# Optimization experiments

Measured on AMD Instinct MI355X. Metric: run time of the kernel, lower is better.

Reference implementation:

```python
import jax, jax.numpy as jnp
import numpy as np

EPS = 1e-6
RATIO = 0.5


def lrelu(x):
    return jnp.where(x > 0, x, 0.1 * x)


def conv1x1(x, w, b):
    # x (B,Ci,H,W), w (Co,Ci)
    return jnp.einsum('bihw,oi->bohw', x, w) + b[None, :, None, None]


def conv3x3(x, w, b, groups=1):
    y = jax.lax.conv_general_dilated(x, w, (1, 1), [(1, 1), (1, 1)],
        dimension_numbers=('NCHW', 'OIHW', 'NCHW'), feature_group_count=groups)
    return y + b[None, :, None, None]


def ln_cf(x, w, b):
    # channels-first LayerNorm over dim 1 (matches custom LayerNorm in source)
    u = x.mean(1, keepdims=True)
    s = ((x - u) ** 2).mean(1, keepdims=True)
    xn = (x - u) / jnp.sqrt(s + EPS)
    return w[None, :, None, None] * xn + b[None, :, None, None]


def flow_warp(x, flow):
    # bilinear warp, align_corners=True, zeros padding; flow (B,H,W,2): ch0=col offset, ch1=row offset (pixels)
    B, C, H, W = x.shape
    sx = jnp.arange(W, dtype=x.dtype)[None, None, :] + flow[..., 0]
    sy = jnp.arange(H, dtype=x.dtype)[None, :, None] + flow[..., 1]
    x0 = jnp.floor(sx)
    y0 = jnp.floor(sy)
    flat = x.reshape(B, C, H * W)

    def gather(xi, yi):
        valid = ((xi >= 0) & (xi <= W - 1) & (yi >= 0) & (yi <= H - 1)).astype(x.dtype)
        xc = jnp.clip(xi, 0, W - 1).astype(jnp.int32)
        yc = jnp.clip(yi, 0, H - 1).astype(jnp.int32)
        idx = (yc * W + xc).reshape(B, H * W)
        g = jnp.take_along_axis(flat, idx[:, None, :], axis=2).reshape(B, C, H, W)
        return g * valid[:, None, :, :]

    wx = sx - x0
    wy = sy - y0
    return (gather(x0, y0) * ((1 - wx) * (1 - wy))[:, None]
            + gather(x0 + 1, y0) * (wx * (1 - wy))[:, None]
            + gather(x0, y0 + 1) * ((1 - wx) * wy)[:, None]
            + gather(x0 + 1, y0 + 1) * (wx * wy)[:, None])


def mixer_forward(x, p_in_w, p_in_b, p_ln_w, p_ln_b, p_off_w1, p_off_b1, p_off_w2, p_off_b2,
                  p_ca_w, p_ca_b, p_sa_w, p_sa_b, p_mask_w1, p_mask_b1, p_mask_w2, p_mask_b2,
                  v_w, v_b, q_w, q_b, k_w, k_b, cs_w, cs_b, out_w, out_b):
    B, C, H, W = x.shape
    N = H * W
    # ---- Predictor (eval path) ----
    gy, gx = jnp.meshgrid(jnp.linspace(-1.0, 1.0, H), jnp.linspace(-1.0, 1.0, W), indexing='ij')
    grid = jnp.broadcast_to(jnp.stack([gx, gy]).astype(x.dtype)[None], (B, 2, H, W))
    cond = jnp.concatenate([x, grid], axis=1)  # (B, C+2, H, W)
    f = lrelu(ln_cf(conv1x1(cond, p_in_w, p_in_b), p_ln_w, p_ln_b))  # (B, (C+2)//4, H, W)
    offsets = jnp.tanh(conv1x1(lrelu(conv1x1(f, p_off_w1, p_off_b1)), p_off_w2, p_off_b2)) * 8.0
    ca = jax.nn.sigmoid(conv1x1(f.mean((2, 3), keepdims=True), p_ca_w, p_ca_b))  # (B,C,1,1)
    sa = jax.nn.sigmoid(conv3x3(f, p_sa_w, p_sa_b))  # (B,1,H,W)
    t = f.mean(1).reshape(B, N, 1)  # window_size=1 -> per-pixel token score input
    s1 = lrelu(t @ p_mask_w1.T + p_mask_b1)
    pred = jax.nn.softmax(s1 @ p_mask_w2.T + p_mask_b2, axis=-1)  # (B,N,2)
    score = pred[..., 0]
    num_keep = int(N * RATIO)  # static keep count (eval-mode deterministic routing)
    idx = jnp.argsort(-score, axis=1)
    idx1, idx2 = idx[:, :num_keep], idx[:, num_keep:]
    # ---- routed mixing ----
    v = conv1x1(x, v_w, v_b)
    k_img = x + flow_warp(x, offsets.transpose(0, 2, 3, 1))
    tok = lambda z: z.reshape(B, C, N).transpose(0, 2, 1)
    q_tok, k_tok, v_tok, vs_tok = tok(x), tok(k_img), tok(v), tok(v * sa)
    sel = lambda z, i: jnp.take_along_axis(z, i[..., None], axis=1)
    q1 = sel(q_tok, idx1) @ q_w.T + q_b
    k1 = sel(k_tok, idx1) @ k_w.T + k_b
    v1 = sel(v_tok, idx1)
    attn = jax.nn.softmax(jnp.einsum('bnc,bmc->bnm', q1, k1) * (C ** -0.5), axis=-1)
    f_attn = jnp.einsum('bnm,bmc->bnc', attn, v1)
    bi = jnp.arange(B)[:, None]
    out_tok = v_tok.at[bi, idx1].set(f_attn).at[bi, idx2].set(sel(vs_tok, idx2))  # batch_index_fill
    out = out_tok.transpose(0, 2, 1).reshape(B, C, H, W)
    out = jax.nn.gelu(conv3x3(out, cs_w, cs_b, groups=C)) * ca + out
    return conv1x1(out, out_w, out_b)


def setup_inputs():
    key = jax.random.key(0)
    ks = iter(jax.random.split(key, 40))
    B, C, H, W = 8, 192, 64, 64
    CD, C4, C8 = C + 2, (C + 2) // 4, (C + 2) // 8

    def w(shape, fan):
        return jax.random.normal(next(ks), shape, jnp.float32) * (fan ** -0.5)

    return dict(
        x=jax.random.normal(next(ks), (B, C, H, W), jnp.float32),
        p_in_w=w((C4, CD), CD), p_in_b=jnp.zeros((C4,)),
        p_ln_w=jnp.ones((C4,)), p_ln_b=jnp.zeros((C4,)),
        p_off_w1=w((C8, C4), C4), p_off_b1=jnp.zeros((C8,)),
        p_off_w2=w((2, C8), C8), p_off_b2=jnp.zeros((2,)),
        p_ca_w=w((C, C4), C4), p_ca_b=jnp.zeros((C,)),
        p_sa_w=w((1, C4, 3, 3), C4 * 9), p_sa_b=jnp.zeros((1,)),
        p_mask_w1=w((1, 1), 1), p_mask_b1=jnp.zeros((1,)),
        p_mask_w2=w((2, 1), 1), p_mask_b2=jnp.zeros((2,)),
        v_w=w((C, C), C), v_b=jnp.zeros((C,)),
        q_w=w((C, C), C), q_b=jnp.zeros((C,)),
        k_w=w((C, C), C), k_b=jnp.zeros((C,)),
        cs_w=w((C, 1, 3, 3), 9), cs_b=jnp.zeros((C,)),
        out_w=w((C, C), C), out_b=jnp.zeros((C,)),
    )


def reference(x, p_in_w, p_in_b, p_ln_w, p_ln_b, p_off_w1, p_off_b1, p_off_w2, p_off_b2,
              p_ca_w, p_ca_b, p_sa_w, p_sa_b, p_mask_w1, p_mask_b1, p_mask_w2, p_mask_b2,
              v_w, v_b, q_w, q_b, k_w, k_b, cs_w, cs_b, out_w, out_b):
    return mixer_forward(x, p_in_w, p_in_b, p_ln_w, p_ln_b, p_off_w1, p_off_b1, p_off_w2, p_off_b2,
                         p_ca_w, p_ca_b, p_sa_w, p_sa_b, p_mask_w1, p_mask_b1, p_mask_w2, p_mask_b2,
                         v_w, v_b, q_w, q_b, k_w, k_b, cs_w, cs_b, out_w, out_b)
```

## Files before the change

### kernel.cpp

```cpp
#include <hip/hip_runtime.h>
#include <hip/hip_bf16.h>

#define NB   8
#define NC   192
#define NH   64
#define NW   64
#define NN   4096
#define NCD  194
#define NC4  48
#define NKEEP 2048
#define NSPLIT 2
#define KPS   (NKEEP/NSPLIT)
#define NT    (KPS/32)

typedef __attribute__((ext_vector_type(8))) short bf16x8;
typedef __attribute__((ext_vector_type(4))) float f32x4;
typedef __hip_bfloat16 bf16;

__device__ __forceinline__ float dsigmoid(float x){ return 1.f/(1.f+__expf(-x)); }
__device__ __forceinline__ float dlrelu(float x){ return x>0.f ? x : 0.1f*x; }
__device__ __forceinline__ float b2f(short s){ return __uint_as_float(((unsigned)(unsigned short)s)<<16); }

__global__ __launch_bounds__(128) void k_f_score(
    const float* __restrict__ x, const float* __restrict__ w_in, const float* __restrict__ b_in,
    const float* __restrict__ ln_w, const float* __restrict__ ln_b,
    const float* __restrict__ mw1, const float* __restrict__ mb1,
    const float* __restrict__ mw2, const float* __restrict__ mb2,
    float* __restrict__ f, float* __restrict__ score)
{
  __shared__ float wT[NCD][NC4];
  int t = threadIdx.x;
  for (int i=t; i<NCD*NC4; i+=128){ int o = i/NCD, c = i - o*NCD; wT[c][o] = w_in[i]; }
  __syncthreads();

  int gid = blockIdx.x*128 + t;
  int p = gid & (NN-1), b = gid >> 12;
  int hh = p>>6, ww = p&63;

  f32x4 a4[12];
  #pragma unroll
  for (int j=0;j<12;++j) a4[j] = *(const f32x4*)(b_in + 4*j);

  const float* xb = x + (size_t)b*NC*NN + p;
  for (int c=0;c<NC;++c){
    float xv = xb[(size_t)c*NN];
    #pragma unroll
    for (int j=0;j<12;++j){ f32x4 wv = *(const f32x4*)&wT[c][4*j]; a4[j] += wv*xv; }
  }
  { float gx = -1.f + (2.f/63.f)*(float)ww;
    #pragma unroll
    for (int j=0;j<12;++j){ f32x4 wv = *(const f32x4*)&wT[192][4*j]; a4[j] += wv*gx; }
    float gy = -1.f + (2.f/63.f)*(float)hh;
    #pragma unroll
    for (int j=0;j<12;++j){ f32x4 wv = *(const f32x4*)&wT[193][4*j]; a4[j] += wv*gy; }
  }
  float s1=0.f, s2=0.f;
  #pragma unroll
  for (int j=0;j<12;++j){
    #pragma unroll
    for (int k=0;k<4;++k){ float v=a4[j][k]; s1+=v; s2+=v*v; }
  }
  float mean = s1*(1.f/NC4);
  float var  = s2*(1.f/NC4) - mean*mean;
  float rstd = rsqrtf(var + 1e-6f);
  float tsum = 0.f;
  #pragma unroll
  for (int j=0;j<12;++j){
    f32x4 lw = *(const f32x4*)(ln_w + 4*j);
    f32x4 lb = *(const f32x4*)(ln_b + 4*j);
    #pragma unroll
    for (int k=0;k<4;++k){
      float z = lw[k]*((a4[j][k]-mean)*rstd) + lb[k];
      float fv = z>0.f ? z : 0.1f*z;
      tsum += fv;
      f[((size_t)b*NC4 + 4*j+k)*NN + p] = fv;
    }
  }
  float tm = tsum*(1.f/NC4);
  float sv = dlrelu(tm*mw1[0] + mb1[0]);
  float d  = sv*(mw2[0]-mw2[1]) + (mb2[0]-mb2[1]);
  score[b*NN + p] = dsigmoid(d);
}

__global__ __launch_bounds__(1024) void k_topk(const float* __restrict__ score,
                                               int* __restrict__ idx1, int* __restrict__ flag)
{
  int b = blockIdx.x;
  int t = threadIdx.x;
  __shared__ unsigned hist[256];
  __shared__ unsigned long long sP;
  __shared__ unsigned sR;
  __shared__ unsigned cnt;
  unsigned long long key[4];
  #pragma unroll
  for (int j=0;j<4;++j){
    int i = t + j*1024;
    unsigned u = __float_as_uint(score[b*NN+i]);
    unsigned a = (u & 0x80000000u) ? ~u : (u | 0x80000000u);
    unsigned d = ~a;
    key[j] = ((unsigned long long)d << 32) | (unsigned)i;
  }
  if (t==0){ sP=0ull; sR=NKEEP-1; cnt=0u; }
  #pragma unroll 1
  for (int pass=0; pass<8; ++pass){
    int shift = 56 - pass*8;
    if (t<256) hist[t]=0u;
    __syncthreads();
    unsigned long long P = sP;
    #pragma unroll
    for (int j=0;j<4;++j){
      bool ok = (pass==0) || ((key[j] >> (shift+8)) == (P >> (shift+8)));
      if (ok) atomicAdd(&hist[(unsigned)((key[j]>>shift)&255ull)], 1u);
    }
    __syncthreads();
    if (t < 64){
      unsigned s[4]; unsigned lsum=0u;
      #pragma unroll
      for (int j=0;j<4;++j){ s[j]=hist[4*t+j]; lsum+=s[j]; }
      unsigned incl = lsum;
      #pragma unroll
      for (int d2=1; d2<64; d2<<=1){
        unsigned v = __shfl_up(incl, d2);
        if (t >= d2) incl += v;
      }
      unsigned before = incl - lsum;
      unsigned R = sR;
      if (R >= before && R < incl){
        unsigned c = before;
        #pragma unroll
        for (int j=0;j<4;++j){
          if (R < c + s[j]){
            sP = sP | ((unsigned long long)(4u*(unsigned)t + (unsigned)j) << shift);
            sR = R - c;
            break;
          }
          c += s[j];
        }
      }
    }
    __syncthreads();
  }
  unsigned long long P = sP;
  #pragma unroll
  for (int j=0;j<4;++j){
    int i = t + j*1024;
    bool sel = (key[j] <= P);
    flag[b*NN+i] = sel ? 1 : 0;
    if (sel){
      unsigned pos = atomicAdd(&cnt, 1u);
      idx1[b*NKEEP + pos] = i;
    }
  }
}

__global__ __launch_bounds__(256) void k_offsets(
    const float* __restrict__ f, const float* __restrict__ w1, const float* __restrict__ b1,
    const float* __restrict__ w2, const float* __restrict__ b2, float* __restrict__ offs)
{
  int gid = blockIdx.x*256 + threadIdx.x;
  int p = gid & (NN-1);
  int b = gid >> 12;
  const float* fb = f + (size_t)b*NC4*NN + p;
  float fl[NC4];
  #pragma unroll 8
  for (int c=0;c<NC4;++c) fl[c] = fb[(size_t)c*NN];
  float h1[24];
  for (int o=0;o<24;++o){
    const float* wr = w1 + o*NC4;
    float a = b1[o];
    #pragma unroll 8
    for (int c=0;c<NC4;++c) a += wr[c]*fl[c];
    h1[o] = dlrelu(a);
  }
  #pragma unroll
  for (int o=0;o<2;++o){
    const float* wr = w2 + o*24;
    float a = b2[o];
    #pragma unroll
    for (int c=0;c<24;++c) a += wr[c]*h1[c];
    offs[((size_t)b*2+o)*NN + p] = tanhf(a)*8.f;
  }
}

__global__ __launch_bounds__(256) void k_fmean(const float* __restrict__ f, float* __restrict__ fmean){
  int bc = blockIdx.x;
  const float* p = f + (size_t)bc*NN;
  float s = 0.f;
  for (int i=threadIdx.x;i<NN;i+=256) s += p[i];
  for (int o=32;o;o>>=1) s += __shfl_xor(s,o);
  __shared__ float r[4];
  if ((threadIdx.x&63)==0) r[threadIdx.x>>6] = s;
  __syncthreads();
  if (threadIdx.x==0) fmean[bc] = (r[0]+r[1]+r[2]+r[3])*(1.f/NN);
}

__global__ void k_ca(const float* __restrict__ fmean, const float* __restrict__ w,
                     const float* __restrict__ bias, float* __restrict__ ca){
  int b = blockIdx.x, o = threadIdx.x;
  const float* fm = fmean + b*NC4;
  float a = bias[o];
  #pragma unroll 8
  for (int c=0;c<NC4;++c) a += w[o*NC4+c]*fm[c];
  ca[b*NC+o] = dsigmoid(a);
}

__global__ __launch_bounds__(256) void k_sa(const float* __restrict__ f, const float* __restrict__ w,
                                            const float* __restrict__ bias, float* __restrict__ sa){
  int hh = blockIdx.x;
  int b  = blockIdx.y;
  __shared__ float fl[3][NC4][66];
  __shared__ float wl[NC4*9];
  __shared__ float ps[4][64];
  int t = threadIdx.x;

  for (int i=t; i<3*NC4*64; i+=256){
    int col = i & 63;
    int rc  = i >> 6;
    int cc  = rc % NC4;
    int rr  = rc / NC4;
    int yy  = hh + rr - 1;
    float v = (yy>=0 && yy<=63) ? f[((size_t)b*NC4+cc)*NN + yy*64 + col] : 0.f;
    fl[rr][cc][1+col] = v;
  }
  if (t < 3*NC4){ int rr=t/NC4, cc=t%NC4; fl[rr][cc][0]=0.f; fl[rr][cc][65]=0.f; }
  for (int i=t; i<NC4*9; i+=256) wl[i] = w[i];
  __syncthreads();

  int ww = t & 63, gq = t >> 6;
  float acc = 0.f;
  #pragma unroll
  for (int j=0;j<12;++j){
    int cc = gq*12 + j;
    const float* wc = &wl[cc*9];
    #pragma unroll
    for (int dy=0;dy<3;++dy){
      acc += fl[dy][cc][ww  ]*wc[dy*3+0];
      acc += fl[dy][cc][ww+1]*wc[dy*3+1];
      acc += fl[dy][cc][ww+2]*wc[dy*3+2];
    }
  }
  ps[gq][ww] = acc;
  __syncthreads();
  if (t < 64){
    float s = ps[0][t]+ps[1][t]+ps[2][t]+ps[3][t] + bias[0];
    sa[(size_t)b*NN + hh*64 + t] = dsigmoid(s);
  }
}

__global__ __launch_bounds__(256) void k_w2bf(const float* __restrict__ a, const float* __restrict__ b,
                                              const float* __restrict__ c, const float* __restrict__ d,
                                              bf16* __restrict__ oa, bf16* __restrict__ ob,
                                              bf16* __restrict__ oc, bf16* __restrict__ od){
  int i = blockIdx.x*256 + threadIdx.x;
  if (i < NC*NC){
    oa[i] = __float2bfloat16(a[i]);
    ob[i] = __float2bfloat16(b[i]);
    oc[i] = __float2bfloat16(c[i]);
    od[i] = __float2bfloat16(d[i]);
  }
}

__global__ __launch_bounds__(256) void k_transpose(const float* __restrict__ in, bf16* __restrict__ outT){
  int b = blockIdx.z;
  int c0 = blockIdx.y*32, p0 = blockIdx.x*32;
  __shared__ float tile[32][33];
  int col = threadIdx.x & 31, row8 = threadIdx.x >> 5;
  #pragma unroll
  for (int ph=0;ph<4;++ph){
    int c = c0 + ph*8 + row8;
    tile[ph*8+row8][col] = in[((size_t)b*NC + c)*NN + p0 + col];
  }
  __syncthreads();
  #pragma unroll
  for (int ph=0;ph<4;++ph){
    int p = p0 + ph*8 + row8;
    outT[((size_t)b*NN + p)*NC + c0 + col] = __float2bfloat16(tile[col][ph*8+row8]);
  }
}

__global__ __launch_bounds__(256) void k_conv_mfma(const bf16* __restrict__ inT, const bf16* __restrict__ wb,
                                                   const float* __restrict__ bias, float* __restrict__ outp,
                                                   const int* __restrict__ flag, const float* __restrict__ sa){
  int b = blockIdx.y;
  int px0 = blockIdx.x*64;
  int wv = threadIdx.x>>6, lane = threadIdx.x&63, g = lane>>4, r = lane&15;
  int o0 = wv*48;
  bf16x8 bw[3][6];
  #pragma unroll
  for (int jo=0;jo<3;++jo)
    #pragma unroll
    for (int ks=0;ks<6;++ks)
      bw[jo][ks] = *(const bf16x8*)(wb + (size_t)(o0+jo*16+r)*NC + ks*32 + 8*g);
  float bv[3];
  #pragma unroll
  for (int jo=0;jo<3;++jo) bv[jo] = bias[o0+jo*16+r];

  const bf16* ib = inT + (size_t)b*NN*NC;
  #pragma unroll
  for (int t=0;t<4;++t){
    int px = px0 + t*16;
    bf16x8 a[6];
    #pragma unroll
    for (int ks=0;ks<6;++ks) a[ks] = *(const bf16x8*)(ib + (size_t)(px+r)*NC + ks*32 + 8*g);
    f32x4 acc[3];
    #pragma unroll
    for (int jo=0;jo<3;++jo){ acc[jo][0]=0.f; acc[jo][1]=0.f; acc[jo][2]=0.f; acc[jo][3]=0.f; }
    #pragma unroll
    for (int ks=0;ks<6;++ks)
      #pragma unroll
      for (int jo=0;jo<3;++jo)
        acc[jo] = __builtin_amdgcn_mfma_f32_16x16x32_bf16(a[ks], bw[jo][ks], acc[jo], 0,0,0);
    float m0=1.f, m1=1.f, m2=1.f, m3=1.f;
    if (flag){
      int pix = px + 4*g;
      int4 f4 = *(const int4*)(flag + (size_t)b*NN + pix);
      float4 s4 = *(const float4*)(sa + (size_t)b*NN + pix);
      m0 = f4.x ? 1.f : s4.x;
      m1 = f4.y ? 1.f : s4.y;
      m2 = f4.z ? 1.f : s4.z;
      m3 = f4.w ? 1.f : s4.w;
    }
    #pragma unroll
    for (int jo=0;jo<3;++jo){
      float4 rv;
      rv.x=(acc[jo][0]+bv[jo])*m0; rv.y=(acc[jo][1]+bv[jo])*m1;
      rv.z=(acc[jo][2]+bv[jo])*m2; rv.w=(acc[jo][3]+bv[jo])*m3;
      *(float4*)(outp + ((size_t)b*NC + o0+jo*16+r)*NN + px + 4*g) = rv;
    }
  }
}

__global__ __launch_bounds__(256) void k_gemm_mfma(const bf16* __restrict__ in, const bf16* __restrict__ wb,
                                                   const float* __restrict__ bias, bf16* __restrict__ outp){
  int b = blockIdx.y;
  int s0 = blockIdx.x*32;
  int wv = threadIdx.x>>6, lane = threadIdx.x&63, g = lane>>4, r = lane&15;
  int o0 = wv*48;
  bf16x8 bw[3][6];
  #pragma unroll
  for (int jo=0;jo<3;++jo)
    #pragma unroll
    for (int ks=0;ks<6;++ks)
      bw[jo][ks] = *(const bf16x8*)(wb + (size_t)(o0+jo*16+r)*NC + ks*32 + 8*g);
  float bv[3];
  #pragma unroll
  for (int jo=0;jo<3;++jo) bv[jo] = bias[o0+jo*16+r];

  const bf16* ib = in + (size_t)b*NKEEP*NC;
  bf16* ob = outp + (size_t)b*NKEEP*NC;
  #pragma unroll
  for (int t=0;t<2;++t){
    int s = s0 + t*16;
    bf16x8 a[6];
    #pragma unroll
    for (int ks=0;ks<6;++ks) a[ks] = *(const bf16x8*)(ib + (size_t)(s+r)*NC + ks*32 + 8*g);
    f32x4 acc[3];
    #pragma unroll
    for (int jo=0;jo<3;++jo){ acc[jo][0]=0.f; acc[jo][1]=0.f; acc[jo][2]=0.f; acc[jo][3]=0.f; }
    #pragma unroll
    for (int ks=0;ks<6;++ks)
      #pragma unroll
      for (int jo=0;jo<3;++jo)
        acc[jo] = __builtin_amdgcn_mfma_f32_16x16x32_bf16(a[ks], bw[jo][ks], acc[jo], 0,0,0);
    #pragma unroll
    for (int jo=0;jo<3;++jo)
      #pragma unroll
      for (int i=0;i<4;++i)
        ob[(size_t)(s+4*g+i)*NC + o0+jo*16+r] = __float2bfloat16(acc[jo][i]+bv[jo]);
  }
}

__global__ __launch_bounds__(256) void k_warp_params(const int* __restrict__ idx1, const float* __restrict__ offs,
                                                     float4* __restrict__ wpar, int4* __restrict__ ipar){
  int gid = blockIdx.x*256 + threadIdx.x;
  int b = gid >> 11;
  int p = idx1[gid];
  int ph = p >> 6, pwx = p & 63;
  float fx = offs[((size_t)b*2+0)*NN + p];
  float fy = offs[((size_t)b*2+1)*NN + p];
  float sx = (float)pwx + fx, sy = (float)ph + fy;
  float x0f = floorf(sx), y0f = floorf(sy);
  float wx = sx - x0f, wy = sy - y0f;
  int x0 = (int)x0f, y0 = (int)y0f;
  bool vx0 = (x0f >= 0.f) && (x0f <= 63.f);
  bool vx1 = (x0f+1.f >= 0.f) && (x0f+1.f <= 63.f);
  bool vy0 = (y0f >= 0.f) && (y0f <= 63.f);
  bool vy1 = (y0f+1.f >= 0.f) && (y0f+1.f <= 63.f);
  int cx0 = min(max(x0,0),63), cx1 = min(max(x0+1,0),63);
  int cy0 = min(max(y0,0),63), cy1 = min(max(y0+1,0),63);
  float4 w4;
  w4.x = (vx0&&vy0) ? (1.f-wx)*(1.f-wy) : 0.f;
  w4.y = (vx1&&vy0) ? wx*(1.f-wy)       : 0.f;
  w4.z = (vx0&&vy1) ? (1.f-wx)*wy       : 0.f;
  w4.w = (vx1&&vy1) ? wx*wy             : 0.f;
  int4 i4;
  i4.x = cy0*64+cx0; i4.y = cy0*64+cx1; i4.z = cy1*64+cx0; i4.w = cy1*64+cx1;
  wpar[gid]=w4; ipar[gid]=i4;
}

__global__ __launch_bounds__(256) void k_gather_qT(const bf16* __restrict__ xT, const int* __restrict__ idx1,
                                                   bf16* __restrict__ qin){
  int gid = blockIdx.x*256 + threadIdx.x;
  int j = gid % 24;
  int bs = gid / 24;
  int b = bs >> 11;
  int p = idx1[bs];
  *(bf16x8*)(qin + (size_t)bs*NC + j*8) = *(const bf16x8*)(xT + ((size_t)b*NN + p)*NC + j*8);
}

__global__ __launch_bounds__(256) void k_gather_kT(const bf16* __restrict__ xT, const int* __restrict__ idx1,
                                                   const float4* __restrict__ wpar, const int4* __restrict__ ipar,
                                                   bf16* __restrict__ kin){
  int gid = blockIdx.x*256 + threadIdx.x;
  int j = gid % 24;
  int bs = gid / 24;
  int b = bs >> 11;
  int p = idx1[bs];
  float4 w4 = wpar[bs]; int4 i4 = ipar[bs];
  const bf16* xb = xT + (size_t)b*NN*NC + j*8;
  bf16x8 v0 = *(const bf16x8*)(xb + (size_t)p*NC);
  bf16x8 v1 = *(const bf16x8*)(xb + (size_t)i4.x*NC);
  bf16x8 v2 = *(const bf16x8*)(xb + (size_t)i4.y*NC);
  bf16x8 v3 = *(const bf16x8*)(xb + (size_t)i4.z*NC);
  bf16x8 v4 = *(const bf16x8*)(xb + (size_t)i4.w*NC);
  bf16x8 o;
  #pragma unroll
  for (int k=0;k<8;++k){
    float vv = b2f(v0[k]) + w4.x*b2f(v1[k]) + w4.y*b2f(v2[k]) + w4.z*b2f(v3[k]) + w4.w*b2f(v4[k]);
    bf16 h = __float2bfloat16(vv);
    o[k] = *(short*)&h;
  }
  *(bf16x8*)(kin + (size_t)bs*NC + j*8) = o;
}

__global__ __launch_bounds__(256) void k_gather_vT(const float* __restrict__ v, const int* __restrict__ idx1,
                                                   bf16* __restrict__ v1T){
  int gid = blockIdx.x*256 + threadIdx.x;
  int s = gid & (NKEEP-1);
  int bc = gid >> 11;
  int b = bc/NC;
  v1T[gid] = __float2bfloat16(v[(size_t)bc*NN + idx1[b*NKEEP+s]]);
}

__global__ __launch_bounds__(256) void k_attn(const bf16* __restrict__ q1, const bf16* __restrict__ k1,
                                              const bf16* __restrict__ v1T,
                                              bf16* __restrict__ pacc, float* __restrict__ pl)
{
  int id = blockIdx.x;
  int b  = id & 7;
  int t2 = id >> 3;
  int sp = t2 & (NSPLIT-1);
  int qb = t2 >> 1;
  int tid = threadIdx.x;
  int wv = tid >> 6;
  int lane = tid & 63;
  int g = lane >> 4, r = lane & 15;
  int q0 = qb*64 + wv*16;

  const bf16* qbp = q1 + (size_t)b*NKEEP*NC;
  const char* kgb = (const char*)(k1 + (size_t)b*NKEEP*NC);
  const char* vgb = (const char*)(v1T + (size_t)b*NC*NKEEP);

  __shared__ __align__(1024) char kl[12288];
  __shared__ __align__(1024) char vl[2][12288];
  __shared__ __align__(16) bf16 plds[4][16][40];
  bf16 (* __restrict__ pw)[40] = plds[wv];
  char* klc = kl;

  int ksrc[3], vsrc[3];
  #pragma unroll
  for (int i=0;i<3;++i){
    int o = (wv*3 + i)*1024 + lane*16;
    int koct = o >> 9;
    int krow = (o >> 4) & 31;
    ksrc[i] = krow*384 + koct*16;
    int voct = o / 3072;
    int vch  = (o - voct*3072) >> 4;
    vsrc[i] = vch*(NKEEP*2) + voct*16;
  }

  const int kbase = sp*KPS;
  auto stage = [&](int k0, int vb){
    char* vlc = vl[vb];
    #pragma unroll
    for (int i=0;i<3;++i){
      int j = wv*3 + i;
      __builtin_amdgcn_global_load_lds(
        (const __attribute__((address_space(1))) void*)(kgb + (size_t)k0*384 + ksrc[i]),
        (__attribute__((address_space(3))) void*)(klc + j*1024), 16, 0, 0);
      __builtin_amdgcn_global_load_lds(
        (const __attribute__((address_space(1))) void*)(vgb + (size_t)k0*2 + vsrc[i]),
        (__attribute__((address_space(3))) void*)(vlc + j*1024), 16, 0, 0);
    }
  };

  bf16x8 aq[6];
  #pragma unroll
  for (int ks=0;ks<6;++ks)
    aq[ks] = *(const bf16x8*)(qbp + (size_t)(q0+r)*NC + 32*ks + 8*g);

  f32x4 acc[12];
  #pragma unroll
  for (int i=0;i<12;++i){ acc[i][0]=0.f; acc[i][1]=0.f; acc[i][2]=0.f; acc[i][3]=0.f; }
  float l[4]={0.f,0.f,0.f,0.f};

  const float scale = 0.07216878364870323f;
  const float shift = 20.f;

  stage(kbase, 0);
  __syncthreads();

  int vb = 0;
  for (int t16=0;t16<NT;++t16) {
    f32x4 s0v, s1v;
    s0v[0]=s0v[1]=s0v[2]=s0v[3]=0.f;
    s1v[0]=s1v[1]=s1v[2]=s1v[3]=0.f;
    #pragma unroll
    for (int ks=0;ks<6;++ks) {
      const char* kp = klc + (size_t)(4*ks+g)*512 + r*16;
      bf16x8 bk0 = *(const bf16x8*)(kp);
      bf16x8 bk1 = *(const bf16x8*)(kp + 256);
      s0v = __builtin_amdgcn_mfma_f32_16x16x32_bf16(aq[ks], bk0, s0v, 0,0,0);
      s1v = __builtin_amdgcn_mfma_f32_16x16x32_bf16(aq[ks], bk1, s1v, 0,0,0);
    }
    #pragma unroll
    for (int i=0;i<4;++i) {
      float e0 = __expf(s0v[i]*scale - shift);
      float e1 = __expf(s1v[i]*scale - shift);
      l[i] += e0 + e1;
      pw[4*g+i][r]    = __float2bfloat16(e0);
      pw[4*g+i][16+r] = __float2bfloat16(e1);
    }
    bf16x8 pa = *(const bf16x8*)(&pw[r][8*g]);

    __syncthreads();
    if (t16+1 < NT) stage(kbase + (t16+1)*32, vb^1);

    const char* vlc = vl[vb];
    #pragma unroll
    for (int ct=0;ct<12;++ct) {
      bf16x8 bvv = *(const bf16x8*)(vlc + g*3072 + (16*ct + r)*16);
      acc[ct] = __builtin_amdgcn_mfma_f32_16x16x32_bf16(pa, bvv, acc[ct], 0,0,0);
    }
    __syncthreads();
    vb ^= 1;
  }

  #pragma unroll
  for (int i=0;i<4;++i){
    #pragma unroll
    for (int o=1;o<16;o<<=1) l[i] += __shfl_xor(l[i],o);
  }
  size_t pbase = (((size_t)(b*32+qb)*NSPLIT + sp)*64);
  if (r==0){
    #pragma unroll
    for (int i=0;i<4;++i) pl[pbase + wv*16 + 4*g + i] = l[i];
  }
  #pragma unroll
  for (int ct=0;ct<12;++ct)
    #pragma unroll
    for (int i=0;i<4;++i)
      pacc[(pbase + wv*16 + 4*g + i)*NC + 16*ct + r] = __float2bfloat16(acc[ct][i]);
}

__global__ __launch_bounds__(256) void k_merge(const bf16* __restrict__ pacc,
                                               const float* __restrict__ pl, const int* __restrict__ idx1,
                                               float* __restrict__ out_img)
{
  int gid = blockIdx.x*256 + threadIdx.x;
  int c = gid % NC;
  int bs = gid / NC;
  int s = bs & (NKEEP-1);
  int b = bs >> 11;
  int qb = s >> 6, ql = s & 63;
  size_t base = ((size_t)(b*32+qb)*NSPLIT)*64 + ql;
  float l = pl[base] + pl[base+64];
  size_t pb = base*NC + c;
  float v = __bfloat162float(pacc[pb])
          + __bfloat162float(pacc[pb + (size_t)64*NC]);
  out_img[((size_t)b*NC + c)*NN + idx1[b*NKEEP + s]] = v / l;
}

__global__ __launch_bounds__(256) void k_dwgelu(const float* __restrict__ vin, const float* __restrict__ ca,
                                                const float* __restrict__ cw, const float* __restrict__ cb,
                                                float* __restrict__ out2){
  int bc = blockIdx.x;
  int c = bc % NC, b = bc / NC;
  __shared__ float tl[66][66];
  int t = threadIdx.x;

  if (t < 66){ tl[0][t] = 0.f; tl[65][t] = 0.f; }
  if (t < 64){ tl[t+1][0] = 0.f; tl[t+1][65] = 0.f; }
  const float* ip = vin + (size_t)bc*NN;
  #pragma unroll
  for (int k=0;k<4;++k){
    int p4 = (t + k*256)*4;
    int hh = p4 >> 6, ww = p4 & 63;
    float4 v4 = *(const float4*)(ip + p4);
    tl[1+hh][1+ww  ] = v4.x;
    tl[1+hh][1+ww+1] = v4.y;
    tl[1+hh][1+ww+2] = v4.z;
    tl[1+hh][1+ww+3] = v4.w;
  }
  float wr[9];
  #pragma unroll
  for (int i=0;i<9;++i) wr[i] = cw[c*9+i];
  float cbv = cb[c];
  float cav = ca[b*NC+c];
  __syncthreads();

  float* op = out2 + (size_t)bc*NN;
  #pragma unroll
  for (int k=0;k<16;++k){
    int p = t + k*256;
    int hh = p >> 6, ww = p & 63;
    float a = cbv;
    #pragma unroll
    for (int dy=0;dy<3;++dy){
      a += tl[hh+dy][ww  ]*wr[dy*3+0];
      a += tl[hh+dy][ww+1]*wr[dy*3+1];
      a += tl[hh+dy][ww+2]*wr[dy*3+2];
    }
    float gl = 0.5f*a*(1.f+tanhf(0.79788456080286536f*(a+0.044715f*a*a*a)));
    op[p] = gl*cav + tl[1+hh][1+ww];
  }
}

extern "C" void kernel_launch(void* const* d_in, const int* in_sizes, int n_in,
                              void* d_out, int out_size, void* d_ws, size_t ws_size,
                              hipStream_t stream)
{
  const float* x       = (const float*)d_in[0];
  const float* p_in_w  = (const float*)d_in[1];
  const float* p_in_b  = (const float*)d_in[2];
  const float* p_ln_w  = (const float*)d_in[3];
  const float* p_ln_b  = (const float*)d_in[4];
  const float* p_off_w1= (const float*)d_in[5];
  const float* p_off_b1= (const float*)d_in[6];
  const float* p_off_w2= (const float*)d_in[7];
  const float* p_off_b2= (const float*)d_in[8];
  const float* p_ca_w  = (const float*)d_in[9];
  const float* p_ca_b  = (const float*)d_in[10];
  const float* p_sa_w  = (const float*)d_in[11];
  const float* p_sa_b  = (const float*)d_in[12];
  const float* p_mask_w1=(const float*)d_in[13];
  const float* p_mask_b1=(const float*)d_in[14];
  const float* p_mask_w2=(const float*)d_in[15];
  const float* p_mask_b2=(const float*)d_in[16];
  const float* v_w     = (const float*)d_in[17];
  const float* v_b     = (const float*)d_in[18];
  const float* q_w     = (const float*)d_in[19];
  const float* q_b     = (const float*)d_in[20];
  const float* k_w     = (const float*)d_in[21];
  const float* k_b     = (const float*)d_in[22];
  const float* cs_w    = (const float*)d_in[23];
  const float* cs_b    = (const float*)d_in[24];
  const float* out_w   = (const float*)d_in[25];
  const float* out_b   = (const float*)d_in[26];
  float* out = (float*)d_out;
  (void)in_sizes; (void)n_in; (void)out_size;

  char* wsp = (char*)d_ws;
  size_t off = 0;
  auto alloc = [&](size_t bytes)->char*{ char* p = wsp + off; off += (bytes + 255) & ~(size_t)255; return p; };
  float* f     = (float*)alloc((size_t)NB*NC4*NN*4);
  float* score = (float*)alloc((size_t)NB*NN*4);
  int*   idx1  = (int*)  alloc((size_t)NB*NKEEP*4);
  int*   flag  = (int*)  alloc((size_t)NB*NN*4);
  float* offs  = (float*)alloc((size_t)NB*2*NN*4);
  float* sa    = (float*)alloc((size_t)NB*NN*4);
  float* fmean = (float*)alloc((size_t)NB*NC4*4);
  float* ca    = (float*)alloc((size_t)NB*NC*4);
  float* vbuf  = (float*)alloc((size_t)NB*NC*NN*4);
  bf16*  q1bf  = (bf16*) alloc((size_t)NB*NKEEP*NC*2);
  bf16*  k1bf  = (bf16*) alloc((size_t)NB*NKEEP*NC*2);
  bf16*  v1T   = (bf16*) alloc((size_t)NB*NC*NKEEP*2);
  float4* wpar = (float4*)alloc((size_t)NB*NKEEP*16);
  int4*   ipar = (int4*) alloc((size_t)NB*NKEEP*16);
  float* out2  = (float*)alloc((size_t)NB*NC*NN*4);
  float* pl    = (float*)alloc((size_t)NB*32*NSPLIT*64*4);
  bf16*  xT    = (bf16*) alloc((size_t)NB*NN*NC*2);
  bf16*  wqb   = (bf16*) alloc((size_t)NC*NC*2);
  bf16*  wkb   = (bf16*) alloc((size_t)NC*NC*2);
  bf16*  wvb   = (bf16*) alloc((size_t)NC*NC*2);
  bf16*  wob   = (bf16*) alloc((size_t)NC*NC*2);
  if (off > ws_size) return;
  bf16* qin  = (bf16*)out2;
  bf16* kin  = qin + (size_t)NB*NKEEP*NC;
  bf16* pacc = (bf16*)out2;
  bf16* out2T = xT;

  k_w2bf<<<(NC*NC+255)/256, 256, 0, stream>>>(q_w, k_w, v_w, out_w, wqb, wkb, wvb, wob);
  k_transpose<<<dim3(NN/32, NC/32, NB), 256, 0, stream>>>(x, xT);
  k_f_score<<<NB*NN/128, 128, 0, stream>>>(x, p_in_w, p_in_b, p_ln_w, p_ln_b,
      p_mask_w1, p_mask_b1, p_mask_w2, p_mask_b2, f, score);
  k_topk<<<NB, 1024, 0, stream>>>(score, idx1, flag);
  k_offsets<<<NB*NN/256, 256, 0, stream>>>(f, p_off_w1, p_off_b1, p_off_w2, p_off_b2, offs);
  k_fmean<<<NB*NC4, 256, 0, stream>>>(f, fmean);
  k_ca<<<NB, NC, 0, stream>>>(fmean, p_ca_w, p_ca_b, ca);
  k_sa<<<dim3(NH, NB), 256, 0, stream>>>(f, p_sa_w, p_sa_b, sa);
  k_conv_mfma<<<dim3(NN/64, NB), 256, 0, stream>>>(xT, wvb, v_b, vbuf, flag, sa);
  k_warp_params<<<NB*NKEEP/256, 256, 0, stream>>>(idx1, offs, wpar, ipar);
  k_gather_qT<<<NB*NKEEP*24/256, 256, 0, stream>>>(xT, idx1, qin);
  k_gather_kT<<<NB*NKEEP*24/256, 256, 0, stream>>>(xT, idx1, wpar, ipar, kin);
  k_gemm_mfma<<<dim3(NKEEP/32, NB), 256, 0, stream>>>(qin, wqb, q_b, q1bf);
  k_gemm_mfma<<<dim3(NKEEP/32, NB), 256, 0, stream>>>(kin, wkb, k_b, k1bf);
  k_gather_vT<<<NB*NC*NKEEP/256, 256, 0, stream>>>(vbuf, idx1, v1T);
  k_attn<<<NB*NSPLIT*32, 256, 0, stream>>>(q1bf, k1bf, v1T, pacc, pl);
  k_merge<<<NB*NKEEP*NC/256, 256, 0, stream>>>(pacc, pl, idx1, vbuf);
  k_dwgelu<<<NB*NC, 256, 0, stream>>>(vbuf, ca, cs_w, cs_b, out2);
  k_transpose<<<dim3(NN/32, NC/32, NB), 256, 0, stream>>>(out2, out2T);
  k_conv_mfma<<<dim3(NN/64, NB), 256, 0, stream>>>(out2T, wob, out_b, out, nullptr, nullptr);
}
```

Measured before the change: 426.8 us.

## Split attention keys four ways, single-buffer V staging, split QK accumulators

Raises the key-split factor of the attention kernel from two to four, doubling the number of blocks to improve GPU occupancy and fill across compute units. V staging drops double-buffering: it becomes a single buffer refilled after the PV MFMAs, with K staged separately, which lowers LDS use per block. The QK dot product is split into two independent accumulator chains to shorten MFMA dependency latency. The merge kernel now sums four partials, which adds partial-output traffic and exposes V load latency because prefetch overlap is reduced.

```diff
diff --git a/kernel.cpp b/kernel.cpp
--- a/kernel.cpp
+++ b/kernel.cpp
@@ -9,7 +9,7 @@
 #define NCD  194
 #define NC4  48
 #define NKEEP 2048
-#define NSPLIT 2
+#define NSPLIT 4
 #define KPS   (NKEEP/NSPLIT)
 #define NT    (KPS/32)
 
@@ -450,7 +450,7 @@
   int b  = id & 7;
   int t2 = id >> 3;
   int sp = t2 & (NSPLIT-1);
-  int qb = t2 >> 1;
+  int qb = t2 >> 2;
   int tid = threadIdx.x;
   int wv = tid >> 6;
   int lane = tid & 63;
@@ -462,10 +462,9 @@
   const char* vgb = (const char*)(v1T + (size_t)b*NC*NKEEP);
 
   __shared__ __align__(1024) char kl[12288];
-  __shared__ __align__(1024) char vl[2][12288];
+  __shared__ __align__(1024) char vl[12288];
   __shared__ __align__(16) bf16 plds[4][16][40];
   bf16 (* __restrict__ pw)[40] = plds[wv];
-  char* klc = kl;
 
   int ksrc[3], vsrc[3];
   #pragma unroll
@@ -480,17 +479,22 @@
   }
 
   const int kbase = sp*KPS;
-  auto stage = [&](int k0, int vb){
-    char* vlc = vl[vb];
+  auto stageK = [&](int k0){
     #pragma unroll
     for (int i=0;i<3;++i){
       int j = wv*3 + i;
       __builtin_amdgcn_global_load_lds(
         (const __attribute__((address_space(1))) void*)(kgb + (size_t)k0*384 + ksrc[i]),
-        (__attribute__((address_space(3))) void*)(klc + j*1024), 16, 0, 0);
+        (__attribute__((address_space(3))) void*)(kl + j*1024), 16, 0, 0);
+    }
+  };
+  auto stageV = [&](int k0){
+    #pragma unroll
+    for (int i=0;i<3;++i){
+      int j = wv*3 + i;
       __builtin_amdgcn_global_load_lds(
         (const __attribute__((address_space(1))) void*)(vgb + (size_t)k0*2 + vsrc[i]),
-        (__attribute__((address_space(3))) void*)(vlc + j*1024), 16, 0, 0);
+        (__attribute__((address_space(3))) void*)(vl + j*1024), 16, 0, 0);
     }
   };
 
@@ -507,22 +511,30 @@
   const float scale = 0.07216878364870323f;
   const float shift = 20.f;
 
-  stage(kbase, 0);
+  stageK(kbase);
+  stageV(kbase);
   __syncthreads();
 
-  int vb = 0;
   for (int t16=0;t16<NT;++t16) {
-    f32x4 s0v, s1v;
-    s0v[0]=s0v[1]=s0v[2]=s0v[3]=0.f;
-    s1v[0]=s1v[1]=s1v[2]=s1v[3]=0.f;
-    #pragma unroll
-    for (int ks=0;ks<6;++ks) {
-      const char* kp = klc + (size_t)(4*ks+g)*512 + r*16;
+    f32x4 s0a, s0b, s1a, s1b;
+    s0a[0]=s0a[1]=s0a[2]=s0a[3]=0.f; s0b=s0a; s1a=s0a; s1b=s0a;
+    #pragma unroll
+    for (int ks=0;ks<3;++ks) {
+      const char* kp = kl + (size_t)(4*ks+g)*512 + r*16;
       bf16x8 bk0 = *(const bf16x8*)(kp);
       bf16x8 bk1 = *(const bf16x8*)(kp + 256);
-      s0v = __builtin_amdgcn_mfma_f32_16x16x32_bf16(aq[ks], bk0, s0v, 0,0,0);
-      s1v = __builtin_amdgcn_mfma_f32_16x16x32_bf16(aq[ks], bk1, s1v, 0,0,0);
-    }
+      s0a = __builtin_amdgcn_mfma_f32_16x16x32_bf16(aq[ks], bk0, s0a, 0,0,0);
+      s1a = __builtin_amdgcn_mfma_f32_16x16x32_bf16(aq[ks], bk1, s1a, 0,0,0);
+    }
+    #pragma unroll
+    for (int ks=3;ks<6;++ks) {
+      const char* kp = kl + (size_t)(4*ks+g)*512 + r*16;
+      bf16x8 bk0 = *(const bf16x8*)(kp);
+      bf16x8 bk1 = *(const bf16x8*)(kp + 256);
+      s0b = __builtin_amdgcn_mfma_f32_16x16x32_bf16(aq[ks], bk0, s0b, 0,0,0);
+      s1b = __builtin_amdgcn_mfma_f32_16x16x32_bf16(aq[ks], bk1, s1b, 0,0,0);
+    }
+    f32x4 s0v = s0a + s0b, s1v = s1a + s1b;
     #pragma unroll
     for (int i=0;i<4;++i) {
       float e0 = __expf(s0v[i]*scale - shift);
@@ -534,16 +546,15 @@
     bf16x8 pa = *(const bf16x8*)(&pw[r][8*g]);
 
     __syncthreads();
-    if (t16+1 < NT) stage(kbase + (t16+1)*32, vb^1);
-
-    const char* vlc = vl[vb];
+    if (t16+1 < NT) stageK(kbase + (t16+1)*32);
+
     #pragma unroll
     for (int ct=0;ct<12;++ct) {
-      bf16x8 bvv = *(const bf16x8*)(vlc + g*3072 + (16*ct + r)*16);
+      bf16x8 bvv = *(const bf16x8*)(vl + g*3072 + (16*ct + r)*16);
       acc[ct] = __builtin_amdgcn_mfma_f32_16x16x32_bf16(pa, bvv, acc[ct], 0,0,0);
     }
     __syncthreads();
-    vb ^= 1;
+    if (t16+1 < NT) stageV(kbase + (t16+1)*32);
   }
 
   #pragma unroll
@@ -574,10 +585,12 @@
   int b = bs >> 11;
   int qb = s >> 6, ql = s & 63;
   size_t base = ((size_t)(b*32+qb)*NSPLIT)*64 + ql;
-  float l = pl[base] + pl[base+64];
+  float l = pl[base] + pl[base+64] + pl[base+128] + pl[base+192];
   size_t pb = base*NC + c;
   float v = __bfloat162float(pacc[pb])
-          + __bfloat162float(pacc[pb + (size_t)64*NC]);
+          + __bfloat162float(pacc[pb + (size_t)64*NC])
+          + __bfloat162float(pacc[pb + (size_t)128*NC])
+          + __bfloat162float(pacc[pb + (size_t)192*NC]);
   out_img[((size_t)b*NC + c)*NN + idx1[b*NKEEP + s]] = v / l;
 }
 
```

New measurement: 420.7 us. No clear change (-1.4%).
